# Performance work log

Hardware: AMD Instinct MI355X
Metric: run time of the kernel (lower is better)

## Reference

```python
import jax, jax.numpy as jnp
import numpy as np

# NVFP4 E2M1 representable magnitudes and decision midpoints (round-to-nearest)
_E2M1_GRID = np.array([0.0, 0.5, 1.0, 1.5, 2.0, 3.0, 4.0, 6.0], dtype=np.float32)
_E2M1_MIDS = np.array([0.25, 0.75, 1.25, 1.75, 2.5, 3.5, 5.0], dtype=np.float32)
_BLOCK = 16  # quant_tile_shape=(1,16)


def fake_quant_nvfp4(t):
    """Blockwise (16 contiguous elems) E2M1 fake quant with pow2 scales."""
    shape = t.shape
    v = t.reshape(-1, _BLOCK)                      # [n_blocks, 16]
    amax = jnp.max(jnp.abs(v), axis=-1, keepdims=True)
    # power-of-2 scale so that amax/scale <= 6 (E2M1 max)
    exp = jnp.ceil(jnp.log2(jnp.maximum(amax, jnp.float32(1e-30)) / 6.0))
    scale = jnp.where(amax > 0, jnp.exp2(exp), jnp.float32(1.0))
    u = v / scale
    a = jnp.abs(u)
    grid = jnp.asarray(_E2M1_GRID, dtype=t.dtype)
    mids = jnp.asarray(_E2M1_MIDS, dtype=t.dtype)
    idx = jnp.digitize(a, mids)                    # nearest E2M1 magnitude index
    q = jnp.sign(u) * grid[idx]
    return (q * scale).reshape(shape)


def setup_inputs() -> dict:
    key = jax.random.key(0)
    kx, kw = jax.random.split(key)
    x = jax.random.normal(kx, (32, 256, 64, 64), dtype=jnp.float32)
    w = jax.random.normal(kw, (256, 256, 3, 3), dtype=jnp.float32) * 0.05
    return {"x": x, "w": w}


def reference(x, w):
    qx = fake_quant_nvfp4(x)
    qw = fake_quant_nvfp4(w)
    # conv2d, stride 1, padding 1, no bias, NCHW / OIHW
    return jax.lax.conv_general_dilated(
        qx, qw,
        window_strides=(1, 1),
        padding=((1, 1), (1, 1)),
        dimension_numbers=("NCHW", "OIHW", "NCHW"),
    )
```

## Files before the change

### kernel.cpp

```cpp
#include <hip/hip_runtime.h>
#include <stdint.h>
#include <stddef.h>

typedef __attribute__((ext_vector_type(8))) short short8;
typedef __attribute__((ext_vector_type(4))) float f32x4;

#define N_IMG 32
#define C_IN  256
#define HH    64
#define WW    64
#define O_OUT 256
#define HP    66
#define WP    66

#define QX_ELEMS (N_IMG*HP*WP*C_IN)
#define QX_BYTES ((size_t)QX_ELEMS*2)
#define QW_ELEMS (9*O_OUT*C_IN)


__device__ __forceinline__ float e2m1_mag(float a) {
    return a < 0.25f ? 0.0f
         : a < 0.75f ? 0.5f
         : a < 1.25f ? 1.0f
         : a < 1.75f ? 1.5f
         : a < 2.5f  ? 2.0f
         : a < 3.5f  ? 3.0f
         : a < 5.0f  ? 4.0f : 6.0f;
}

__device__ __forceinline__ void blk_scale2(float amax, float& s, float& inv) {
    float ac = fmaxf(amax, 1e-30f);
    int e;
    float m = frexpf(ac, &e);
    int ex = (m > 0.75f) ? (e - 2) : (e - 3);
    if (amax > 0.0f) { s = ldexpf(1.0f, ex); inv = ldexpf(1.0f, -ex); }
    else             { s = 1.0f; inv = 1.0f; }
}

__device__ __forceinline__ unsigned short to_bf16_bits(float v) {
    union { float f; unsigned int u; } cv; cv.f = v;
    return (unsigned short)(cv.u >> 16);
}

__global__ __launch_bounds__(256) void halo_zero_kernel(unsigned short* __restrict__ qx) {
    int id = blockIdx.x * 256 + threadIdx.x;
    size_t off;
    if (id < 135168) {
        int n = id / 4224, r = id % 4224;
        int h = (r / 2112) * 65;
        int k = r % 2112;
        off = (((size_t)(n*HP + h)) * WP) * C_IN + (size_t)k * 8;
    } else {
        int j = id - 135168;
        int n = j >> 12, r = j & 4095;
        int h = 1 + (r >> 6);
        int w = ((r >> 5) & 1) * 65;
        int k = r & 31;
        off = (((size_t)(n*HP + h)) * WP + w) * C_IN + (size_t)k * 8;
    }
    uint4 z; z.x = z.y = z.z = z.w = 0u;
    *(uint4*)(qx + off) = z;
}

__global__ __launch_bounds__(256) void quant_x_kernel(const float* __restrict__ x,
                                                      unsigned short* __restrict__ qx) {
    __shared__ unsigned short xq[64][66];

    const int bid = blockIdx.x;
    const int n = bid >> 6;
    const int h = bid & 63;
    const int t = threadIdx.x;
    const int c_l = t >> 2;
    const int wq  = t & 3;
    const int wr  = t & 63;
    const int cg  = (t >> 6) * 16;

    const float* srcb = x + (((size_t)(n*C_IN + c_l)) * HH + h) * WW + wq*16;
    unsigned short* dstb = qx + (((size_t)(n*HP + h + 1)) * WP + (wr + 1)) * C_IN + cg;

    for (int cb = 0; cb < 4; ++cb) {
        const float* src = srcb + (size_t)(cb*64) * (HH*WW);
        float v[16];
#pragma unroll
        for (int j = 0; j < 4; ++j) {
            float4 f = ((const float4*)src)[j];
            v[j*4+0]=f.x; v[j*4+1]=f.y; v[j*4+2]=f.z; v[j*4+3]=f.w;
        }
        float amax = 0.f;
#pragma unroll
        for (int k = 0; k < 16; ++k) amax = fmaxf(amax, fabsf(v[k]));
        float s, inv;
        blk_scale2(amax, s, inv);
#pragma unroll
        for (int k = 0; k < 8; ++k) {
            unsigned short lo = to_bf16_bits(copysignf(e2m1_mag(fabsf(v[2*k])   * inv) * s, v[2*k]));
            unsigned short hi = to_bf16_bits(copysignf(e2m1_mag(fabsf(v[2*k+1]) * inv) * s, v[2*k+1]));
            *(unsigned int*)&xq[c_l][wq*16 + 2*k] = ((unsigned int)hi << 16) | (unsigned int)lo;
        }
        __syncthreads();
        unsigned short outv[16];
#pragma unroll
        for (int i = 0; i < 16; ++i) outv[i] = xq[cg + i][wr];
        unsigned short* dst = dstb + cb*64;
        *(uint4*)(dst)     = *(const uint4*)&outv[0];
        *(uint4*)(dst + 8) = *(const uint4*)&outv[8];
        __syncthreads();
    }
}

__global__ __launch_bounds__(256) void quant_w_kernel(const float* __restrict__ w,
                                                      unsigned short* __restrict__ qw) {
    __shared__ unsigned short lq[2304];
    const int o = blockIdx.x;
    const int t = threadIdx.x;
    const float* src = w + (size_t)o * 2304;
    if (t < 144) {
        float v[16];
#pragma unroll
        for (int j = 0; j < 4; ++j) {
            float4 f = ((const float4*)(src + t*16))[j];
            v[j*4+0]=f.x; v[j*4+1]=f.y; v[j*4+2]=f.z; v[j*4+3]=f.w;
        }
        float amax = 0.f;
#pragma unroll
        for (int j = 0; j < 16; ++j) amax = fmaxf(amax, fabsf(v[j]));
        float s, inv;
        blk_scale2(amax, s, inv);
#pragma unroll
        for (int j = 0; j < 16; ++j)
            lq[t*16 + j] = to_bf16_bits(copysignf(e2m1_mag(fabsf(v[j]) * inv) * s, v[j]));
    }
    __syncthreads();
#pragma unroll
    for (int p = 0; p < 9; ++p)
        qw[((size_t)(p*O_OUT + o)) * C_IN + t] = lq[t*9 + p];
}

__device__ __forceinline__ void gld16(void* lds, const void* g) {
    __builtin_amdgcn_global_load_lds(
        (const __attribute__((address_space(1))) unsigned int*)g,
        (__attribute__((address_space(3))) unsigned int*)lds,
        16, 0, 0);
}

__device__ __forceinline__ short8 rd8(const void* p) {
    return *(const short8*)p;
}

#define MFMA16 __builtin_amdgcn_mfma_f32_16x16x32_bf16

#define MM16(I0, A00, A01, A10, A11, B)                                   \
    do {                                                                  \
        _Pragma("unroll")                                                 \
        for (int j = 0; j < 4; ++j) {                                     \
            acc[I0][j]     = MFMA16(A00, B[j][0], acc[I0][j],     0,0,0); \
            acc[I0][j]     = MFMA16(A01, B[j][1], acc[I0][j],     0,0,0); \
            acc[(I0)+1][j] = MFMA16(A10, B[j][0], acc[(I0)+1][j], 0,0,0); \
            acc[(I0)+1][j] = MFMA16(A11, B[j][1], acc[(I0)+1][j], 0,0,0); \
        }                                                                 \
    } while (0)

#define RDQB(D0, D1, D2, D3, BASE, Q)                                     \
    D0 = rd8((BASE) + rA + (2*(Q))*2048   + cA0);                         \
    D1 = rd8((BASE) + rA + (2*(Q))*2048   + (cA0^64));                    \
    D2 = rd8((BASE) + rA + (2*(Q)+1)*2048 + cA0);                         \
    D3 = rd8((BASE) + rA + (2*(Q)+1)*2048 + (cA0^64));

#define PH_OPEN()                                                         \
    __builtin_amdgcn_s_barrier();                                         \
    asm volatile("s_waitcnt lgkmcnt(0)" ::: "memory");                    \
    __builtin_amdgcn_sched_barrier(0);                                    \
    __builtin_amdgcn_s_setprio(1);

#define PH_CLOSE(VM)                                                      \
    __builtin_amdgcn_s_setprio(0);                                        \
    asm volatile("s_waitcnt " VM ::: "memory");                           \
    __builtin_amdgcn_s_barrier();

#define CONV_TILE(TN, LAOFF, BCUR, BNXT)                                  \
    do {                                                                  \
        const int tn  = (TN);                                             \
        const int pn  = tn >> 2;                                          \
        const int qn  = pn / 3;                                           \
        const int dwn = pn - qn * 3;                                      \
        const int cn  = (tn & 3) << 6;                                    \
        const unsigned short* ga = gA + pn * 65536 + cn;                  \
        const unsigned short* gb = gB + (ptrdiff_t)((qn - 1) * WP + (dwn - 1)) * C_IN + cn; \
        const char* LA = Lc + (LAOFF);                                    \
        char* SA = Lc + ((LAOFF) ^ 65536);                                \
        char* SB = SA + 32768;                                            \
         \
        gld16(SB + bwb,         gb);                                      \
        gld16(SB + bwb + 8192,  gb + 16896);                              \
        gld16(SB + bwb + 16384, gb + 2*16896);                            \
        gld16(SB + bwb + 24576, gb + 3*16896);                            \
        PH_OPEN();                                                        \
        RDQB(aB0, aB1, aB2, aB3, LA, 1);                                  \
        MM16(0, aA0, aA1, aA2, aA3, BCUR);                                \
        PH_CLOSE("vmcnt(5)");                                             \
                   \
        gld16(SA + awb,        ga);                                       \
        gld16(SA + awb + 4096, ga + 8192);                                \
        PH_OPEN();                                                        \
        RDQB(aA0, aA1, aA2, aA3, LA, 2);                                  \
        MM16(2, aB0, aB1, aB2, aB3, BCUR);                                \
        PH_CLOSE("vmcnt(6)");                                             \
                   \
        gld16(SA + awb + 8192,  ga + 16384);                              \
        gld16(SA + awb + 12288, ga + 24576);                              \
        PH_OPEN();                                                        \
        RDQB(aB0, aB1, aB2, aB3, LA, 3);                                  \
        MM16(4, aA0, aA1, aA2, aA3, BCUR);                                \
        PH_CLOSE("vmcnt(3)");                                             \
         \
        PH_OPEN();                                                        \
        _Pragma("unroll")                                                 \
        for (int j = 0; j < 4; ++j) {                                     \
            BNXT[j][0] = rd8(SB + rB + j*2048 + cA0);                     \
            BNXT[j][1] = rd8(SB + rB + j*2048 + (cA0^64));                \
        }                                                                 \
        RDQB(aA0, aA1, aA2, aA3, SA, 0);                                  \
        MM16(6, aB0, aB1, aB2, aB3, BCUR);                                \
        PH_CLOSE("vmcnt(2)");                                             \
    } while (0)

__global__ __launch_bounds__(512) void conv_kernel(const unsigned short* __restrict__ qw,
                                                   const unsigned short* __restrict__ qx,
                                                   float* __restrict__ out) {
    __shared__ unsigned short lds[65536];
    char* Lc = (char*)lds;

    const int tid  = threadIdx.x;
    const int w    = tid >> 6;
    const int lane = tid & 63;
    const int lo16 = lane & 15;
    const int quad = lane >> 4;
    const int wm   = w & 1;
    const int wn   = w >> 1;

    const int id  = blockIdx.x;
    const int idx = id >> 3;
    const int n   = (id & 7) + ((idx >> 4) << 3);
    const int pt  = idx & 15;
    const int h0  = pt * 4;
    const int hw0 = pt * 256;

    const int trow  = tid >> 3;
    const int c_off = ((tid & 7) ^ (trow & 7)) << 3;
    const unsigned short* gB = qx + ((size_t)((n*HP + h0 + 1) * WP + trow + 1)) * C_IN + c_off;
    const int ro0 = trow + ((tid >= 256) ? 96 : 0);
    const unsigned short* gA = qw + (size_t)ro0 * C_IN + c_off;
    const int awb = w * 1024 + ((w < 4) ? 0 : 12288);
    const int bwb = w * 1024;

    const int key = (lo16 & 7) << 4;
    const int cA0 = (quad << 4) ^ key;
    const int rA  = (wm * 128 + lo16) * 128;
    const int rB  = (wn * 64  + lo16) * 128;

    f32x4 acc[8][4];
#pragma unroll
    for (int i = 0; i < 8; ++i)
#pragma unroll
        for (int j = 0; j < 4; ++j)
            acc[i][j] = (f32x4){0.f, 0.f, 0.f, 0.f};

    {
        const unsigned short* ga = gA;
        const unsigned short* gb = gB - 17152;
        char* SA = Lc;
        char* SB = Lc + 32768;
        gld16(SB + bwb,         gb);
        gld16(SB + bwb + 8192,  gb + 16896);
        gld16(SB + bwb + 16384, gb + 2*16896);
        gld16(SB + bwb + 24576, gb + 3*16896);
        gld16(SA + awb,         ga);
        gld16(SA + awb + 4096,  ga + 8192);
        gld16(SA + awb + 8192,  ga + 16384);
        gld16(SA + awb + 12288, ga + 24576);
        asm volatile("s_waitcnt vmcnt(0)" ::: "memory");
        __builtin_amdgcn_s_barrier();
    }

    short8 aA0, aA1, aA2, aA3, aB0, aB1, aB2, aB3;
    short8 b0[4][2], b1[4][2];
    {
        const char* LB = Lc + 32768;
#pragma unroll
        for (int j = 0; j < 4; ++j) {
            b0[j][0] = rd8(LB + rB + j*2048 + cA0);
            b0[j][1] = rd8(LB + rB + j*2048 + (cA0^64));
        }
        const char* LA = Lc;
        RDQB(aA0, aA1, aA2, aA3, LA, 0);
    }

#pragma unroll 1
    for (int tt = 0; tt < 18; ++tt) {
        const int t0 = tt * 2;
        CONV_TILE(t0 + 1, 0, b0, b1);
        CONV_TILE((t0 + 2 < 36) ? (t0 + 2) : 35, 65536, b1, b0);
    }

    asm volatile("s_waitcnt vmcnt(0)" ::: "memory");

#pragma unroll
    for (int i = 0; i < 8; ++i) {
        const int o = wm * 128 + i * 16 + quad * 4;
        float* orow = out + ((size_t)(n * O_OUT + o)) * (HH*WW) + hw0 + wn * 64 + lo16;
#pragma unroll
        for (int j = 0; j < 4; ++j) {
            float* dst = orow + j * 16;
#pragma unroll
            for (int r = 0; r < 4; ++r)
                dst[(size_t)r * (HH*WW)] = acc[i][j][r];
        }
    }
}

extern "C" void kernel_launch(void* const* d_in, const int* in_sizes, int n_in,
                              void* d_out, int out_size, void* d_ws, size_t ws_size,
                              hipStream_t stream) {
    const float* x = (const float*)d_in[0];
    const float* w = (const float*)d_in[1];
    float* out = (float*)d_out;

    unsigned short* qx = (unsigned short*)d_ws;
    unsigned short* qw = (unsigned short*)((char*)d_ws + QX_BYTES);

    halo_zero_kernel<<<dim3(1040), 256, 0, stream>>>(qx);
    quant_x_kernel<<<dim3(N_IMG*HH), 256, 0, stream>>>(x, qx);
    quant_w_kernel<<<dim3(O_OUT), 256, 0, stream>>>(w, qw);
    conv_kernel<<<dim3(512), 512, 0, stream>>>(qw, qx, out);
}
```

Measured before the change: 358.8 us.

## Fuse weight quant with halo zeroing, restructure x quant transpose, drop phase barrier

Merges the halo-zero and weight-quant kernels into one launch to save a kernel launch. The x quantization is restructured so each thread handles a full channel row with a single LDS pass and an XOR-swizzled layout, removing the per-channel-block loop and its repeated barriers. It also removes the s_barrier at the start of each conv phase, leaving one barrier per phase, which cuts synchronisation but depends on the remaining waitcnt and barrier placement to keep LDS reuse safe.

After: 357.7 us. No clear change (-0.3%).

```diff
diff --git a/kernel.cpp b/kernel.cpp
--- a/kernel.cpp
+++ b/kernel.cpp
@@ -42,48 +42,24 @@
     return (unsigned short)(cv.u >> 16);
 }
 
-__global__ __launch_bounds__(256) void halo_zero_kernel(unsigned short* __restrict__ qx) {
-    int id = blockIdx.x * 256 + threadIdx.x;
-    size_t off;
-    if (id < 135168) {
-        int n = id / 4224, r = id % 4224;
-        int h = (r / 2112) * 65;
-        int k = r % 2112;
-        off = (((size_t)(n*HP + h)) * WP) * C_IN + (size_t)k * 8;
-    } else {
-        int j = id - 135168;
-        int n = j >> 12, r = j & 4095;
-        int h = 1 + (r >> 6);
-        int w = ((r >> 5) & 1) * 65;
-        int k = r & 31;
-        off = (((size_t)(n*HP + h)) * WP + w) * C_IN + (size_t)k * 8;
-    }
-    uint4 z; z.x = z.y = z.z = z.w = 0u;
-    *(uint4*)(qx + off) = z;
-}
-
 __global__ __launch_bounds__(256) void quant_x_kernel(const float* __restrict__ x,
                                                       unsigned short* __restrict__ qx) {
-    __shared__ unsigned short xq[64][66];
+    __shared__ unsigned int xq[8192];
+    unsigned short* xq16 = (unsigned short*)xq;
 
     const int bid = blockIdx.x;
-    const int n = bid >> 6;
-    const int h = bid & 63;
+    const int n = bid >> 6, h = bid & 63;
     const int t = threadIdx.x;
-    const int c_l = t >> 2;
-    const int wq  = t & 3;
-    const int wr  = t & 63;
-    const int cg  = (t >> 6) * 16;
-
-    const float* srcb = x + (((size_t)(n*C_IN + c_l)) * HH + h) * WW + wq*16;
-    unsigned short* dstb = qx + (((size_t)(n*HP + h + 1)) * WP + (wr + 1)) * C_IN + cg;
-
-    for (int cb = 0; cb < 4; ++cb) {
-        const float* src = srcb + (size_t)(cb*64) * (HH*WW);
+
+    const float* src = x + (((size_t)(n*C_IN + t)) * HH + h) * WW;
+    const int dbase = t >> 1, half = t & 1;
+
+#pragma unroll
+    for (int b = 0; b < 4; ++b) {
         float v[16];
 #pragma unroll
         for (int j = 0; j < 4; ++j) {
-            float4 f = ((const float4*)src)[j];
+            float4 f = ((const float4*)src)[b*4 + j];
             v[j*4+0]=f.x; v[j*4+1]=f.y; v[j*4+2]=f.z; v[j*4+3]=f.w;
         }
         float amax = 0.f;
@@ -92,27 +68,54 @@
         float s, inv;
         blk_scale2(amax, s, inv);
 #pragma unroll
-        for (int k = 0; k < 8; ++k) {
-            unsigned short lo = to_bf16_bits(copysignf(e2m1_mag(fabsf(v[2*k])   * inv) * s, v[2*k]));
-            unsigned short hi = to_bf16_bits(copysignf(e2m1_mag(fabsf(v[2*k+1]) * inv) * s, v[2*k+1]));
-            *(unsigned int*)&xq[c_l][wq*16 + 2*k] = ((unsigned int)hi << 16) | (unsigned int)lo;
-        }
-        __syncthreads();
-        unsigned short outv[16];
-#pragma unroll
-        for (int i = 0; i < 16; ++i) outv[i] = xq[cg + i][wr];
-        unsigned short* dst = dstb + cb*64;
-        *(uint4*)(dst)     = *(const uint4*)&outv[0];
-        *(uint4*)(dst + 8) = *(const uint4*)&outv[8];
-        __syncthreads();
-    }
-}
-
-__global__ __launch_bounds__(256) void quant_w_kernel(const float* __restrict__ w,
-                                                      unsigned short* __restrict__ qw) {
+        for (int k = 0; k < 16; ++k) {
+            const int wrow = b*16 + k;
+            unsigned short qv = to_bf16_bits(copysignf(e2m1_mag(fabsf(v[k]) * inv) * s, v[k]));
+            const int d = dbase ^ ((wrow & 7) << 2);
+            xq16[wrow*256 + d*2 + half] = qv;
+        }
+    }
+    __syncthreads();
+
+    const int pix = t >> 2, seg = t & 3;
+    unsigned short* dst = qx + (((size_t)(n*HP + h + 1)) * WP + (pix + 1)) * C_IN + seg*64;
+    const unsigned int* rowp = xq + pix*128;
+    const int px7 = pix & 7;
+#pragma unroll
+    for (int r = 0; r < 8; ++r) {
+        const int gs = (seg*8 + r) ^ px7;
+        uint4 d4 = *(const uint4*)(rowp + gs*4);
+        *(uint4*)(dst + r*8) = d4;
+    }
+}
+
+__global__ __launch_bounds__(256) void quant_w_halo_kernel(const float* __restrict__ w,
+                                                           unsigned short* __restrict__ qw,
+                                                           unsigned short* __restrict__ qx) {
+    const int b = blockIdx.x;
+    const int t = threadIdx.x;
+    if (b >= O_OUT) {
+        int id = (b - O_OUT) * 256 + t;
+        size_t off;
+        if (id < 135168) {
+            int n = id / 4224, r = id % 4224;
+            int h = (r / 2112) * 65;
+            int k = r % 2112;
+            off = (((size_t)(n*HP + h)) * WP) * C_IN + (size_t)k * 8;
+        } else {
+            int j = id - 135168;
+            int n = j >> 12, r = j & 4095;
+            int h = 1 + (r >> 6);
+            int ww = ((r >> 5) & 1) * 65;
+            int k = r & 31;
+            off = (((size_t)(n*HP + h)) * WP + ww) * C_IN + (size_t)k * 8;
+        }
+        uint4 z; z.x = z.y = z.z = z.w = 0u;
+        *(uint4*)(qx + off) = z;
+        return;
+    }
     __shared__ unsigned short lq[2304];
-    const int o = blockIdx.x;
-    const int t = threadIdx.x;
+    const int o = b;
     const float* src = w + (size_t)o * 2304;
     if (t < 144) {
         float v[16];
@@ -166,13 +169,12 @@
     D2 = rd8((BASE) + rA + (2*(Q)+1)*2048 + cA0);                         \
     D3 = rd8((BASE) + rA + (2*(Q)+1)*2048 + (cA0^64));
 
-#define PH_OPEN()                                                         \
-    __builtin_amdgcn_s_barrier();                                         \
+#define PH_START()                                                        \
     asm volatile("s_waitcnt lgkmcnt(0)" ::: "memory");                    \
     __builtin_amdgcn_sched_barrier(0);                                    \
     __builtin_amdgcn_s_setprio(1);
 
-#define PH_CLOSE(VM)                                                      \
+#define PH_BOUND(VM)                                                      \
     __builtin_amdgcn_s_setprio(0);                                        \
     asm volatile("s_waitcnt " VM ::: "memory");                           \
     __builtin_amdgcn_s_barrier();
@@ -194,26 +196,26 @@
         gld16(SB + bwb + 8192,  gb + 16896);                              \
         gld16(SB + bwb + 16384, gb + 2*16896);                            \
         gld16(SB + bwb + 24576, gb + 3*16896);                            \
-        PH_OPEN();                                                        \
+        PH_START();                                                       \
         RDQB(aB0, aB1, aB2, aB3, LA, 1);                                  \
         MM16(0, aA0, aA1, aA2, aA3, BCUR);                                \
-        PH_CLOSE("vmcnt(5)");                                             \
+        PH_BOUND("vmcnt(5)");                                             \
                    \
         gld16(SA + awb,        ga);                                       \
         gld16(SA + awb + 4096, ga + 8192);                                \
-        PH_OPEN();                                                        \
+        PH_START();                                                       \
         RDQB(aA0, aA1, aA2, aA3, LA, 2);                                  \
         MM16(2, aB0, aB1, aB2, aB3, BCUR);                                \
-        PH_CLOSE("vmcnt(6)");                                             \
+        PH_BOUND("vmcnt(6)");                                             \
                    \
         gld16(SA + awb + 8192,  ga + 16384);                              \
         gld16(SA + awb + 12288, ga + 24576);                              \
-        PH_OPEN();                                                        \
+        PH_START();                                                       \
         RDQB(aB0, aB1, aB2, aB3, LA, 3);                                  \
         MM16(4, aA0, aA1, aA2, aA3, BCUR);                                \
-        PH_CLOSE("vmcnt(3)");                                             \
+        PH_BOUND("vmcnt(3)");                                             \
          \
-        PH_OPEN();                                                        \
+        PH_START();                                                       \
         _Pragma("unroll")                                                 \
         for (int j = 0; j < 4; ++j) {                                     \
             BNXT[j][0] = rd8(SB + rB + j*2048 + cA0);                     \
@@ -221,7 +223,7 @@
         }                                                                 \
         RDQB(aA0, aA1, aA2, aA3, SA, 0);                                  \
         MM16(6, aB0, aB1, aB2, aB3, BCUR);                                \
-        PH_CLOSE("vmcnt(2)");                                             \
+        PH_BOUND("vmcnt(2)");                                             \
     } while (0)
 
 __global__ __launch_bounds__(512) void conv_kernel(const unsigned short* __restrict__ qw,
@@ -328,8 +330,7 @@
     unsigned short* qx = (unsigned short*)d_ws;
     unsigned short* qw = (unsigned short*)((char*)d_ws + QX_BYTES);
 
-    halo_zero_kernel<<<dim3(1040), 256, 0, stream>>>(qx);
+    quant_w_halo_kernel<<<dim3(O_OUT + 1040), 256, 0, stream>>>(w, qw, qx);
     quant_x_kernel<<<dim3(N_IMG*HH), 256, 0, stream>>>(x, qx);
-    quant_w_kernel<<<dim3(O_OUT), 256, 0, stream>>>(w, qw);
     conv_kernel<<<dim3(512), 512, 0, stream>>>(qw, qx, out);
 }
```
